# Performance work log

Measured on AMD Instinct MI355X. Metric: run time of the kernel, lower is better.

Reference implementation:

```python
import jax, jax.numpy as jnp
import numpy as np

N_NODES = 100000
N_EDGES = 1600000
D_IN = 128
D_H = 128
NUM_GRAPHS = 128


def setup_inputs() -> dict:
    key = jax.random.key(0)
    ks = jax.random.split(key, 16)
    x = jax.random.normal(ks[0], (N_NODES, D_IN), dtype=jnp.float32)
    edge_index = jax.random.randint(ks[1], (2, N_EDGES), 0, N_NODES, dtype=jnp.int64)
    batch_index = jnp.sort(jax.random.randint(ks[2], (N_NODES,), 0, NUM_GRAPHS, dtype=jnp.int64))
    s = 0.05
    W1 = s * jax.random.normal(ks[3], (D_IN, D_H), dtype=jnp.float32)
    b1 = jnp.zeros((D_H,), jnp.float32)
    W2 = s * jax.random.normal(ks[4], (D_H, D_H), dtype=jnp.float32)
    b2 = jnp.zeros((D_H,), jnp.float32)
    W3 = s * jax.random.normal(ks[5], (D_H, D_H), dtype=jnp.float32)
    b3 = jnp.zeros((D_H,), jnp.float32)
    W4 = s * jax.random.normal(ks[6], (D_H, D_H), dtype=jnp.float32)
    b4 = jnp.zeros((D_H,), jnp.float32)
    Wl = s * jax.random.normal(ks[7], (2 * D_H, 1), dtype=jnp.float32)
    bl = jnp.zeros((1,), jnp.float32)
    return {"x": x, "edge_index": edge_index, "batch_index": batch_index,
            "W1": W1, "b1": b1, "W2": W2, "b2": b2, "W3": W3, "b3": b3,
            "W4": W4, "b4": b4, "Wl": Wl, "bl": bl}


def _gcn_prep(edge_index, n_nodes):
    # add self-loops, symmetric normalization D^-1/2 (A+I) D^-1/2
    loops = jnp.arange(n_nodes, dtype=edge_index.dtype)
    row = jnp.concatenate([edge_index[0], loops])  # source
    col = jnp.concatenate([edge_index[1], loops])  # target
    deg = jax.ops.segment_sum(jnp.ones_like(col, dtype=jnp.float32), col,
                              num_segments=n_nodes)
    dinv = jnp.where(deg > 0, jax.lax.rsqrt(jnp.maximum(deg, 1.0)), 0.0)
    norm = dinv[row] * dinv[col]  # [E+N]
    return row, col, norm


def _gcn(h, W, b, row, col, norm, n_nodes):
    h = h @ W                                   # [N, H]
    msg = h[row] * norm[:, None]                # gather + scale
    return jax.ops.segment_sum(msg, col, num_segments=n_nodes) + b


def reference(x, edge_index, batch_index, W1, b1, W2, b2, W3, b3, W4, b4, Wl, bl):
    n = x.shape[0]
    row, col, norm = _gcn_prep(edge_index, n)
    h = jnp.tanh(_gcn(x, W1, b1, row, col, norm, n))
    h = jnp.tanh(_gcn(h, W2, b2, row, col, norm, n))
    h = jnp.tanh(_gcn(h, W3, b3, row, col, norm, n))
    h = jnp.tanh(_gcn(h, W4, b4, row, col, norm, n))
    # global max / mean pool per graph
    cnt = jax.ops.segment_sum(jnp.ones((n,), jnp.float32), batch_index,
                              num_segments=NUM_GRAPHS)
    mx = jax.ops.segment_max(h, batch_index, num_segments=NUM_GRAPHS)
    mx = jnp.where(cnt[:, None] > 0, mx, 0.0)
    sm = jax.ops.segment_sum(h, batch_index, num_segments=NUM_GRAPHS)
    mn = sm / jnp.maximum(cnt, 1.0)[:, None]
    pooled = jnp.concatenate([mx, mn], axis=1)  # [G, 2H]
    return pooled @ Wl + bl                     # [G, 1]
```

## Files before the change

kernel.cpp:

```cpp
#include <hip/hip_runtime.h>
#include <hip/hip_bf16.h>
#include <math.h>

#define PSPLIT 8
#define BSH 5
#define BW 32
#define AST 40

typedef float v4f __attribute__((ext_vector_type(4)));
typedef unsigned int v4u __attribute__((ext_vector_type(4)));
typedef unsigned int v2u __attribute__((ext_vector_type(2)));
typedef __attribute__((ext_vector_type(8))) short bf8;
typedef __attribute__((ext_vector_type(4))) float f4;
typedef unsigned short u16;
typedef unsigned int u32;

static inline size_t align_up(size_t x, size_t a){ return (x + a - 1) & ~(a - 1); }

__device__ inline void bf_split(float v, u16& hi, u16& lo){
  __hip_bfloat16 h = __float2bfloat16(v);
  float hf = __bfloat162float(h);
  __hip_bfloat16 l = __float2bfloat16(v - hf);
  hi = *(u16*)&h; lo = *(u16*)&l;
}

__device__ inline void fmixlo(float& a, u32 p){
  asm("v_fma_mix_f32 %0, %1, 1.0, %0 op_sel:[0,0,0] op_sel_hi:[1,0,0]" : "+v"(a) : "v"(p));
}
__device__ inline void fmixhi(float& a, u32 p){
  asm("v_fma_mix_f32 %0, %1, 1.0, %0 op_sel:[1,0,0] op_sel_hi:[1,0,0]" : "+v"(a) : "v"(p));
}


__global__ __launch_bounds__(256) void k_bhist(const int* __restrict__ col, int* __restrict__ bcnt,
                                               int E, int NB,
                                               const int* __restrict__ batch, int* __restrict__ gstart,
                                               int n, int G){
  extern __shared__ int lh[];
  for (int i = threadIdx.x; i < NB; i += 256) lh[i] = 0;
  __syncthreads();
  for (int e = blockIdx.x * 256 + threadIdx.x; e < E; e += gridDim.x * 256)
    atomicAdd(&lh[col[e] >> BSH], 1);
  __syncthreads();
  for (int i = threadIdx.x; i < NB; i += 256){
    int v = lh[i];
    if (v) atomicAdd(&bcnt[i], v);
  }
  for (int i = blockIdx.x * 256 + threadIdx.x; i < n; i += gridDim.x * 256){
    int cb = batch[i];
    if (i == 0){ for (int g = 0; g <= cb; ++g) gstart[g] = 0; }
    else { int pb = batch[i - 1]; for (int g = pb + 1; g <= cb; ++g) gstart[g] = i; }
    if (i == n - 1){ for (int g = cb + 1; g <= G; ++g) gstart[g] = n; }
  }
}

__global__ void k_bscan(const int* __restrict__ bcnt, int* __restrict__ boff, int NB, int E,
                        int* __restrict__ rp, int N){
  __shared__ int sd[256];
  int t = threadIdx.x;
  int c[16]; int s = 0;
  const int PT = (NB + 255) / 256;
  for (int j = 0; j < PT; ++j){ int i = t * PT + j; c[j] = (i < NB) ? bcnt[i] : 0; s += c[j]; }
  sd[t] = s; __syncthreads();
  for (int off = 1; off < 256; off <<= 1){
    int v = sd[t];
    if (t >= off) v += sd[t - off];
    __syncthreads(); sd[t] = v; __syncthreads();
  }
  int run = sd[t] - s;
  for (int j = 0; j < PT; ++j){ int i = t * PT + j; if (i < NB) boff[i] = run; run += c[j]; }
  if (t == 255){ boff[NB] = run; rp[N] = E; }
}

__global__ __launch_bounds__(256) void k_bscat(const int* __restrict__ ei, const int* __restrict__ boff,
                                               int* __restrict__ bfill, unsigned* __restrict__ tmp, int E){
  int e = blockIdx.x * 256 + threadIdx.x;
  if (e >= E) return;
  int s = ei[e], d = ei[E + e];
  int b = d >> BSH;
  int p = atomicAdd(&bfill[b * 32], 1);
  tmp[boff[b] + p] = (unsigned)s | ((unsigned)(d & (BW - 1)) << 17);
}

__global__ __launch_bounds__(256) void k_bfin(const unsigned* __restrict__ tmp, const int* __restrict__ boff,
                                              int* __restrict__ ssrc, int* __restrict__ rp,
                                              float* __restrict__ dinv, int N){
  int b = blockIdx.x;
  int d0 = b << BSH;
  int lim = N - d0; if (lim > BW) lim = BW;
  __shared__ int dcnt[BW], dst_[BW], lfill[BW];
  int t = threadIdx.x;
  if (t < BW){ dcnt[t] = 0; lfill[t] = 0; }
  __syncthreads();
  int lo = boff[b], hi = boff[b + 1];
  for (int i = lo + t; i < hi; i += 256) atomicAdd(&dcnt[tmp[i] >> 17], 1);
  __syncthreads();
  if (t == 0){ int run = 0; for (int l = 0; l < BW; ++l){ dst_[l] = run; run += dcnt[l]; } }
  __syncthreads();
  if (t < lim){
    int d = d0 + t;
    rp[d] = lo + dst_[t];
    double dd = (double)(dcnt[t] + 1);
    dinv[d] = (float)(1.0 / sqrt(dd));
  }
  __syncthreads();
  for (int i = lo + t; i < hi; i += 256){
    unsigned r = tmp[i];
    int l = r >> 17;
    int pos = dst_[l] + atomicAdd(&lfill[l], 1);
    ssrc[lo + pos] = (int)(r & 0x1FFFFu);
  }
}


__global__ __launch_bounds__(256) void k_cvtw(const float* __restrict__ w0, const float* __restrict__ w1,
                                              const float* __restrict__ w2, const float* __restrict__ w3,
                                              u16* __restrict__ wth, u16* __restrict__ wtl){
  int id = blockIdx.x * 256 + threadIdx.x;
  if (id >= 4 * 16384) return;
  int l = id >> 14, rem = id & 16383, k = rem >> 7, nn = rem & 127;
  const float* Wsrc = (l == 0) ? w0 : (l == 1) ? w1 : (l == 2) ? w2 : w3;
  float v = Wsrc[k * 128 + nn];
  u16 hi, lo; bf_split(v, hi, lo);
  wth[(l << 14) + nn * 128 + k] = hi;
  wtl[(l << 14) + nn * 128 + k] = lo;
}


__global__ __launch_bounds__(256, 4) void k_gemm(const float* __restrict__ A,
                                                 const u16* __restrict__ wth, const u16* __restrict__ wtl,
                                                 const float* __restrict__ dinv,
                                                 u16* __restrict__ C, int n, int packed){
  __shared__ u16 Ah[128 * AST], Al[128 * AST], Wh[128 * AST], Wl[128 * AST];
  int t = threadIdx.x;
  int r0 = blockIdx.x * 128;
  int wv = t >> 6, lane = t & 63;
  int q = lane >> 4, ln = lane & 15;

  int srow = t >> 1;
  int shalf = (t & 1) * 16;
  int grow = r0 + srow; if (grow > n - 1) grow = n - 1;
  const float* ga = A + (size_t)grow * 128 + shalf;
  const u16* gwh = wth + srow * 128 + shalf;
  const u16* gwl = wtl + srow * 128 + shalf;

  f4 acc[2][8];
  #pragma unroll
  for (int mt = 0; mt < 2; ++mt)
    #pragma unroll
    for (int nt = 0; nt < 8; ++nt) acc[mt][nt] = (f4)(0.f);

  for (int c = 0; c < 4; ++c){
    __syncthreads();
    {
      u16* ah = &Ah[srow * AST + shalf];
      u16* al = &Al[srow * AST + shalf];
      if (packed){
        const v4u* gp = (const v4u*)(ga + c * 32);
        #pragma unroll
        for (int i = 0; i < 4; ++i){
          v4u v = gp[i];
          ushort4 hv = {(u16)(v.x >> 16), (u16)(v.y >> 16), (u16)(v.z >> 16), (u16)(v.w >> 16)};
          ushort4 lv = {(u16)v.x, (u16)v.y, (u16)v.z, (u16)v.w};
          *(ushort4*)&ah[i * 4] = hv;
          *(ushort4*)&al[i * 4] = lv;
        }
      } else {
        const float4* gp = (const float4*)(ga + c * 32);
        #pragma unroll
        for (int i = 0; i < 4; ++i){
          float4 v = gp[i];
          u16 h0,h1,h2,h3,l0,l1,l2,l3;
          bf_split(v.x, h0, l0); bf_split(v.y, h1, l1);
          bf_split(v.z, h2, l2); bf_split(v.w, h3, l3);
          ushort4 hv = {h0,h1,h2,h3}, lv = {l0,l1,l2,l3};
          *(ushort4*)&ah[i * 4] = hv;
          *(ushort4*)&al[i * 4] = lv;
        }
      }
    }
    {
      const u16* ph = gwh + c * 32;
      const u16* pl = gwl + c * 32;
      bf8 h0 = *(const bf8*)ph, h1 = *(const bf8*)(ph + 8);
      bf8 l0 = *(const bf8*)pl, l1 = *(const bf8*)(pl + 8);
      *(bf8*)&Wh[srow * AST + shalf] = h0; *(bf8*)&Wh[srow * AST + shalf + 8] = h1;
      *(bf8*)&Wl[srow * AST + shalf] = l0; *(bf8*)&Wl[srow * AST + shalf + 8] = l1;
    }
    __syncthreads();

    bf8 afh[2], afl[2];
    #pragma unroll
    for (int mt = 0; mt < 2; ++mt){
      int row = wv * 32 + mt * 16 + ln;
      afh[mt] = *(const bf8*)&Ah[row * AST + q * 8];
      afl[mt] = *(const bf8*)&Al[row * AST + q * 8];
    }
    #pragma unroll
    for (int nt = 0; nt < 8; ++nt){
      int wn = nt * 16 + ln;
      bf8 wfh = *(const bf8*)&Wh[wn * AST + q * 8];
      bf8 wfl = *(const bf8*)&Wl[wn * AST + q * 8];
      #pragma unroll
      for (int mt = 0; mt < 2; ++mt){
        acc[mt][nt] = __builtin_amdgcn_mfma_f32_16x16x32_bf16(afh[mt], wfh, acc[mt][nt], 0, 0, 0);
        acc[mt][nt] = __builtin_amdgcn_mfma_f32_16x16x32_bf16(afl[mt], wfh, acc[mt][nt], 0, 0, 0);
        acc[mt][nt] = __builtin_amdgcn_mfma_f32_16x16x32_bf16(afh[mt], wfl, acc[mt][nt], 0, 0, 0);
      }
    }
  }

  #pragma unroll
  for (int mt = 0; mt < 2; ++mt){
    int base_m = r0 + wv * 32 + mt * 16 + q * 4;
    float dv[4];
    #pragma unroll
    for (int reg = 0; reg < 4; ++reg){
      int row = base_m + reg;
      dv[reg] = (row < n) ? dinv[row] : 0.f;
    }
    #pragma unroll
    for (int nt = 0; nt < 8; ++nt){
      #pragma unroll
      for (int reg = 0; reg < 4; ++reg){
        int row = base_m + reg;
        if (row < n){
          _Float16 hv = (_Float16)(acc[mt][nt][reg] * dv[reg]);
          C[(size_t)row * 128 + nt * 16 + ln] = *(u16*)&hv;
        }
      }
    }
  }
}


__global__ __launch_bounds__(256) void k_agg(const u16* __restrict__ hwp, const int* __restrict__ rp,
                                             const int* __restrict__ ssrc,
                                             const float* __restrict__ dinv, const float* __restrict__ bias,
                                             float* __restrict__ hout, int n, int pack){
  int b = blockIdx.x;
  int r = b & 7;
  int F = r >> 2;
  int s = (b >> 3) * 4 + (r & 3);
  int node = s * 4 + (threadIdx.x >> 6);
  if (node >= n) return;
  int lane = threadIdx.x & 63;
  int ql = lane >> 4;
  int fl = lane & 15;
  const char* hbase = (const char*)(hwp + F * 64);
  u32 flb = (u32)fl * 8;

  int e0 = rp[node], e1 = rp[node + 1];
  float a0 = 0.f, a1 = 0.f, a2 = 0.f, a3 = 0.f;
  for (int eb = e0; eb < e1; eb += 64){
    int m = e1 - eb; if (m > 64) m = 64;
    int sl = (lane < m) ? ssrc[eb + lane] : 0;
    int mp = m & ~3;
    int j = 0;
    for (; j + 16 <= mp; j += 16){
      int s0 = __shfl(sl, j + ql),     s1 = __shfl(sl, j + 4 + ql);
      int s2 = __shfl(sl, j + 8 + ql), s3 = __shfl(sl, j + 12 + ql);
      v2u v0 = *(const v2u*)(hbase + (((u32)s0 << 8) + flb));
      v2u v1 = *(const v2u*)(hbase + (((u32)s1 << 8) + flb));
      v2u v2_ = *(const v2u*)(hbase + (((u32)s2 << 8) + flb));
      v2u v3 = *(const v2u*)(hbase + (((u32)s3 << 8) + flb));
      fmixlo(a0, v0.x); fmixhi(a1, v0.x); fmixlo(a2, v0.y); fmixhi(a3, v0.y);
      fmixlo(a0, v1.x); fmixhi(a1, v1.x); fmixlo(a2, v1.y); fmixhi(a3, v1.y);
      fmixlo(a0, v2_.x); fmixhi(a1, v2_.x); fmixlo(a2, v2_.y); fmixhi(a3, v2_.y);
      fmixlo(a0, v3.x); fmixhi(a1, v3.x); fmixlo(a2, v3.y); fmixhi(a3, v3.y);
    }
    if (j + 8 <= mp){
      int s0 = __shfl(sl, j + ql), s1 = __shfl(sl, j + 4 + ql);
      v2u v0 = *(const v2u*)(hbase + (((u32)s0 << 8) + flb));
      v2u v1 = *(const v2u*)(hbase + (((u32)s1 << 8) + flb));
      fmixlo(a0, v0.x); fmixhi(a1, v0.x); fmixlo(a2, v0.y); fmixhi(a3, v0.y);
      fmixlo(a0, v1.x); fmixhi(a1, v1.x); fmixlo(a2, v1.y); fmixhi(a3, v1.y);
      j += 8;
    }
    if (j + 4 <= mp){
      int s0 = __shfl(sl, j + ql);
      v2u v0 = *(const v2u*)(hbase + (((u32)s0 << 8) + flb));
      fmixlo(a0, v0.x); fmixhi(a1, v0.x); fmixlo(a2, v0.y); fmixhi(a3, v0.y);
      j += 4;
    }
    if (j < m){
      int s0 = __shfl(sl, j + ql);
      if (j + ql < m){
        v2u v0 = *(const v2u*)(hbase + (((u32)s0 << 8) + flb));
        fmixlo(a0, v0.x); fmixhi(a1, v0.x); fmixlo(a2, v0.y); fmixhi(a3, v0.y);
      }
    }
  }
  a0 += __shfl_down(a0, 32); a1 += __shfl_down(a1, 32);
  a2 += __shfl_down(a2, 32); a3 += __shfl_down(a3, 32);
  a0 += __shfl_down(a0, 16); a1 += __shfl_down(a1, 16);
  a2 += __shfl_down(a2, 16); a3 += __shfl_down(a3, 16);
  if (lane < 16){
    v2u sv = *(const v2u*)(hbase + (((u32)node << 8) + flb));
    fmixlo(a0, sv.x); fmixhi(a1, sv.x); fmixlo(a2, sv.y); fmixhi(a3, sv.y);
    float di = dinv[node];
    int f = F * 64 + fl * 4;
    v4f bv = *(const v4f*)(bias + f);
    float r0 = tanhf(a0 * di + bv.x);
    float r1 = tanhf(a1 * di + bv.y);
    float r2 = tanhf(a2 * di + bv.z);
    float r3 = tanhf(a3 * di + bv.w);
    if (pack){
      u16 h0,h1,h2,h3,l0,l1,l2,l3;
      bf_split(r0, h0, l0); bf_split(r1, h1, l1);
      bf_split(r2, h2, l2); bf_split(r3, h3, l3);
      v4u pv;
      pv.x = ((u32)h0 << 16) | l0; pv.y = ((u32)h1 << 16) | l1;
      pv.z = ((u32)h2 << 16) | l2; pv.w = ((u32)h3 << 16) | l3;
      __builtin_nontemporal_store(pv, (v4u*)(hout + (size_t)node * 128 + f));
    } else {
      v4f rr; rr.x = r0; rr.y = r1; rr.z = r2; rr.w = r3;
      __builtin_nontemporal_store(rr, (v4f*)(hout + (size_t)node * 128 + f));
    }
  }
}


__global__ __launch_bounds__(256) void k_pool1(const float* __restrict__ h, const int* __restrict__ gstart,
                                               float* __restrict__ pmx, float* __restrict__ psm){
  int g = blockIdx.x >> 3, s = blockIdx.x & (PSPLIT - 1);
  int t = threadIdx.x;
  int fq = t & 31;
  int rw = t >> 5;
  int i0 = gstart[g], i1 = gstart[g + 1];
  int len = i1 - i0;
  int chunk = (len + PSPLIT - 1) / PSPLIT;
  int a = i0 + s * chunk;
  int b = a + chunk; if (b > i1) b = i1;

  const v4f* hv = (const v4f*)h;
  v4f mx = (v4f)(-INFINITY), sm = (v4f)(0.f);
  for (int i = a + rw; i < b; i += 8){
    v4f v = hv[(size_t)i * 32 + fq];
    mx.x = fmaxf(mx.x, v.x); mx.y = fmaxf(mx.y, v.y);
    mx.z = fmaxf(mx.z, v.z); mx.w = fmaxf(mx.w, v.w);
    sm += v;
  }
  __shared__ v4f smx[8][32], ssm[8][32];
  smx[rw][fq] = mx; ssm[rw][fq] = sm;
  __syncthreads();
  if (rw == 0){
    #pragma unroll
    for (int r2 = 1; r2 < 8; ++r2){
      v4f m2 = smx[r2][fq], s2 = ssm[r2][fq];
      mx.x = fmaxf(mx.x, m2.x); mx.y = fmaxf(mx.y, m2.y);
      mx.z = fmaxf(mx.z, m2.z); mx.w = fmaxf(mx.w, m2.w);
      sm += s2;
    }
    ((v4f*)pmx)[(size_t)blockIdx.x * 32 + fq] = mx;
    ((v4f*)psm)[(size_t)blockIdx.x * 32 + fq] = sm;
  }
}

__global__ __launch_bounds__(128) void k_head(const float* __restrict__ pmx, const float* __restrict__ psm,
                                              const int* __restrict__ gstart,
                                              const float* __restrict__ Wl, const float* __restrict__ bl,
                                              float* __restrict__ out){
  int g = blockIdx.x, f = threadIdx.x;
  float mx = -INFINITY, sm = 0.f;
  #pragma unroll
  for (int s = 0; s < PSPLIT; ++s){
    mx = fmaxf(mx, pmx[((size_t)g * PSPLIT + s) * 128 + f]);
    sm += psm[((size_t)g * PSPLIT + s) * 128 + f];
  }
  int cnt = gstart[g + 1] - gstart[g];
  if (cnt <= 0) mx = 0.f;
  float mn = sm / (float)(cnt > 0 ? cnt : 1);
  float contrib = mx * Wl[f] + mn * Wl[128 + f];
  for (int o = 32; o > 0; o >>= 1) contrib += __shfl_down(contrib, o);
  __shared__ float sred[2];
  if ((f & 63) == 0) sred[f >> 6] = contrib;
  __syncthreads();
  if (f == 0) out[g] = sred[0] + sred[1] + bl[0];
}


extern "C" void kernel_launch(void* const* d_in, const int* in_sizes, int n_in,
                              void* d_out, int out_size, void* d_ws, size_t ws_size,
                              hipStream_t stream){
  const float* x     = (const float*)d_in[0];
  const int*   ei    = (const int*)d_in[1];
  const int*   batch = (const int*)d_in[2];
  const float* W[4]  = {(const float*)d_in[3], (const float*)d_in[5], (const float*)d_in[7], (const float*)d_in[9]};
  const float* B[4]  = {(const float*)d_in[4], (const float*)d_in[6], (const float*)d_in[8], (const float*)d_in[10]};
  const float* Wl    = (const float*)d_in[11];
  const float* bl    = (const float*)d_in[12];
  float* out = (float*)d_out;

  int N = in_sizes[0] / 128;
  int E = in_sizes[1] / 2;
  int G = out_size;
  int NB = (N + BW - 1) >> BSH;

  char* ws = (char*)d_ws;
  size_t off = 0;
  auto alloc = [&](size_t bytes) -> void* {
    void* p = ws + off; off = align_up(off + bytes, 256); return p;
  };
  float* dinv  = (float*)alloc((size_t)N * 4);
  int*   rp    = (int*)  alloc((size_t)(N + 1) * 4);
  int*   bcnt  = (int*)  alloc((size_t)(NB + 1) * 4);
  int*   boff  = (int*)  alloc((size_t)(NB + 1) * 4);
  int*   bfill = (int*)  alloc((size_t)NB * 32 * 4);
  int*   gst   = (int*)  alloc((size_t)(G + 1) * 4);
  int*   ssrc  = (int*)  alloc((size_t)E * 4);
  u16*   wth   = (u16*)  alloc((size_t)4 * 16384 * 2);
  u16*   wtl   = (u16*)  alloc((size_t)4 * 16384 * 2);
  float* pmx   = (float*)alloc((size_t)G * PSPLIT * 128 * 4);
  float* psm   = (float*)alloc((size_t)G * PSPLIT * 128 * 4);
  u16*   hw    = (u16*)  alloc((size_t)N * 128 * 2);
  float* h     = (float*)alloc((size_t)N * 128 * 4);
  unsigned* tmp = (unsigned*)hw;

  hipMemsetAsync(bcnt, 0, (size_t)(NB + 1) * 4, stream);
  hipMemsetAsync(bfill, 0, (size_t)NB * 32 * 4, stream);

  int gE = (E + 255) / 256;
  k_cvtw <<<256, 256, 0, stream>>>(W[0], W[1], W[2], W[3], wth, wtl);
  k_bhist<<<128, 256, NB * 4, stream>>>(ei + E, bcnt, E, NB, batch, gst, N, G);
  k_bscan<<<1, 256, 0, stream>>>(bcnt, boff, NB, E, rp, N);
  k_bscat<<<gE, 256, 0, stream>>>(ei, boff, bfill, tmp, E);
  k_bfin <<<NB, 256, 0, stream>>>(tmp, boff, ssrc, rp, dinv, N);

  int gemmG = (N + 127) / 128;
  int slots = (N + 3) / 4;
  int aggG  = 8 * ((slots + 3) / 4);
  const float* hin = x;
  for (int l = 0; l < 4; ++l){
    k_gemm<<<gemmG, 256, 0, stream>>>(hin, wth + (l << 14), wtl + (l << 14), dinv, hw, N, l > 0);
    k_agg <<<aggG, 256, 0, stream>>>(hw, rp, ssrc, dinv, B[l], h, N, l < 3);
    hin = h;
  }
  k_pool1<<<G * PSPLIT, 256, 0, stream>>>(h, gst, pmx, psm);
  k_head <<<G, 128, 0, stream>>>(pmx, psm, gst, Wl, bl, out);
}
```

Baseline: 655.0 us.

## Restructure aggregation to one wave per node over all features with fast tanh

The aggregation kernel now assigns one 64-lane wave to each node, with every lane covering two features of the full 128-wide row. Previously sixteen lanes each covered four features of one 64-feature half, and four edge groups ran in parallel and were combined by shuffle reductions. The new layout removes the feature split across blocks, the shuffle-based index broadcast and the reductions. Neighbour indices are read as wave-uniform scalar loads, and edges are unrolled by 16 to keep many row gathers in flight. tanhf is replaced by an exp2/rcp approximation, which is cheaper but may lose some accuracy and could overflow for large inputs.

After: 579.6 us. 1.13x faster.

```diff
diff --git a/kernel.cpp b/kernel.cpp
--- a/kernel.cpp
+++ b/kernel.cpp
@@ -8,6 +8,7 @@
 #define AST 40
 
 typedef float v4f __attribute__((ext_vector_type(4)));
+typedef float v2f __attribute__((ext_vector_type(2)));
 typedef unsigned int v4u __attribute__((ext_vector_type(4)));
 typedef unsigned int v2u __attribute__((ext_vector_type(2)));
 typedef __attribute__((ext_vector_type(8))) short bf8;
@@ -29,6 +30,12 @@
 }
 __device__ inline void fmixhi(float& a, u32 p){
   asm("v_fma_mix_f32 %0, %1, 1.0, %0 op_sel:[1,0,0] op_sel_hi:[1,0,0]" : "+v"(a) : "v"(p));
+}
+
+__device__ inline float tanh_fast(float x){
+  float u = __builtin_amdgcn_exp2f(x * 2.8853900817779268f);
+  float q = __builtin_amdgcn_rcpf(u + 1.0f);
+  return fmaf(-2.0f, q, 1.0f);
 }
 
 
@@ -238,85 +245,61 @@
                                              const int* __restrict__ ssrc,
                                              const float* __restrict__ dinv, const float* __restrict__ bias,
                                              float* __restrict__ hout, int n, int pack){
-  int b = blockIdx.x;
-  int r = b & 7;
-  int F = r >> 2;
-  int s = (b >> 3) * 4 + (r & 3);
-  int node = s * 4 + (threadIdx.x >> 6);
+  int node = blockIdx.x * 4 + (threadIdx.x >> 6);
+  node = __builtin_amdgcn_readfirstlane(node);
   if (node >= n) return;
   int lane = threadIdx.x & 63;
-  int ql = lane >> 4;
-  int fl = lane & 15;
-  const char* hbase = (const char*)(hwp + F * 64);
-  u32 flb = (u32)fl * 8;
+  const u32* hw32 = (const u32*)hwp;
 
   int e0 = rp[node], e1 = rp[node + 1];
-  float a0 = 0.f, a1 = 0.f, a2 = 0.f, a3 = 0.f;
-  for (int eb = e0; eb < e1; eb += 64){
-    int m = e1 - eb; if (m > 64) m = 64;
-    int sl = (lane < m) ? ssrc[eb + lane] : 0;
-    int mp = m & ~3;
-    int j = 0;
-    for (; j + 16 <= mp; j += 16){
-      int s0 = __shfl(sl, j + ql),     s1 = __shfl(sl, j + 4 + ql);
-      int s2 = __shfl(sl, j + 8 + ql), s3 = __shfl(sl, j + 12 + ql);
-      v2u v0 = *(const v2u*)(hbase + (((u32)s0 << 8) + flb));
-      v2u v1 = *(const v2u*)(hbase + (((u32)s1 << 8) + flb));
-      v2u v2_ = *(const v2u*)(hbase + (((u32)s2 << 8) + flb));
-      v2u v3 = *(const v2u*)(hbase + (((u32)s3 << 8) + flb));
-      fmixlo(a0, v0.x); fmixhi(a1, v0.x); fmixlo(a2, v0.y); fmixhi(a3, v0.y);
-      fmixlo(a0, v1.x); fmixhi(a1, v1.x); fmixlo(a2, v1.y); fmixhi(a3, v1.y);
-      fmixlo(a0, v2_.x); fmixhi(a1, v2_.x); fmixlo(a2, v2_.y); fmixhi(a3, v2_.y);
-      fmixlo(a0, v3.x); fmixhi(a1, v3.x); fmixlo(a2, v3.y); fmixhi(a3, v3.y);
-    }
-    if (j + 8 <= mp){
-      int s0 = __shfl(sl, j + ql), s1 = __shfl(sl, j + 4 + ql);
-      v2u v0 = *(const v2u*)(hbase + (((u32)s0 << 8) + flb));
-      v2u v1 = *(const v2u*)(hbase + (((u32)s1 << 8) + flb));
-      fmixlo(a0, v0.x); fmixhi(a1, v0.x); fmixlo(a2, v0.y); fmixhi(a3, v0.y);
-      fmixlo(a0, v1.x); fmixhi(a1, v1.x); fmixlo(a2, v1.y); fmixhi(a3, v1.y);
-      j += 8;
-    }
-    if (j + 4 <= mp){
-      int s0 = __shfl(sl, j + ql);
-      v2u v0 = *(const v2u*)(hbase + (((u32)s0 << 8) + flb));
-      fmixlo(a0, v0.x); fmixhi(a1, v0.x); fmixlo(a2, v0.y); fmixhi(a3, v0.y);
-      j += 4;
-    }
-    if (j < m){
-      int s0 = __shfl(sl, j + ql);
-      if (j + ql < m){
-        v2u v0 = *(const v2u*)(hbase + (((u32)s0 << 8) + flb));
-        fmixlo(a0, v0.x); fmixhi(a1, v0.x); fmixlo(a2, v0.y); fmixhi(a3, v0.y);
-      }
-    }
-  }
-  a0 += __shfl_down(a0, 32); a1 += __shfl_down(a1, 32);
-  a2 += __shfl_down(a2, 32); a3 += __shfl_down(a3, 32);
-  a0 += __shfl_down(a0, 16); a1 += __shfl_down(a1, 16);
-  a2 += __shfl_down(a2, 16); a3 += __shfl_down(a3, 16);
-  if (lane < 16){
-    v2u sv = *(const v2u*)(hbase + (((u32)node << 8) + flb));
-    fmixlo(a0, sv.x); fmixhi(a1, sv.x); fmixlo(a2, sv.y); fmixhi(a3, sv.y);
-    float di = dinv[node];
-    int f = F * 64 + fl * 4;
-    v4f bv = *(const v4f*)(bias + f);
-    float r0 = tanhf(a0 * di + bv.x);
-    float r1 = tanhf(a1 * di + bv.y);
-    float r2 = tanhf(a2 * di + bv.z);
-    float r3 = tanhf(a3 * di + bv.w);
-    if (pack){
-      u16 h0,h1,h2,h3,l0,l1,l2,l3;
-      bf_split(r0, h0, l0); bf_split(r1, h1, l1);
-      bf_split(r2, h2, l2); bf_split(r3, h3, l3);
-      v4u pv;
-      pv.x = ((u32)h0 << 16) | l0; pv.y = ((u32)h1 << 16) | l1;
-      pv.z = ((u32)h2 << 16) | l2; pv.w = ((u32)h3 << 16) | l3;
-      __builtin_nontemporal_store(pv, (v4u*)(hout + (size_t)node * 128 + f));
-    } else {
-      v4f rr; rr.x = r0; rr.y = r1; rr.z = r2; rr.w = r3;
-      __builtin_nontemporal_store(rr, (v4f*)(hout + (size_t)node * 128 + f));
-    }
+  float a0 = 0.f, a1 = 0.f;
+  int e = e0;
+  while (e + 16 <= e1){
+    u32 p[16];
+    #pragma unroll
+    for (int i = 0; i < 16; ++i){
+      int s = ssrc[e + i];
+      p[i] = hw32[(size_t)s * 64 + lane];
+    }
+    #pragma unroll
+    for (int i = 0; i < 16; ++i){ fmixlo(a0, p[i]); fmixhi(a1, p[i]); }
+    e += 16;
+  }
+  while (e + 4 <= e1){
+    u32 p[4];
+    #pragma unroll
+    for (int i = 0; i < 4; ++i){
+      int s = ssrc[e + i];
+      p[i] = hw32[(size_t)s * 64 + lane];
+    }
+    #pragma unroll
+    for (int i = 0; i < 4; ++i){ fmixlo(a0, p[i]); fmixhi(a1, p[i]); }
+    e += 4;
+  }
+  while (e < e1){
+    int s = ssrc[e];
+    u32 p = hw32[(size_t)s * 64 + lane];
+    fmixlo(a0, p); fmixhi(a1, p);
+    ++e;
+  }
+  {
+    u32 p = hw32[(size_t)node * 64 + lane];
+    fmixlo(a0, p); fmixhi(a1, p);
+  }
+  float di = dinv[node];
+  v2f bv = *(const v2f*)(bias + lane * 2);
+  float r0 = tanh_fast(fmaf(a0, di, bv.x));
+  float r1 = tanh_fast(fmaf(a1, di, bv.y));
+  if (pack){
+    u16 h0, h1, l0, l1;
+    bf_split(r0, h0, l0); bf_split(r1, h1, l1);
+    v2u pv;
+    pv.x = ((u32)h0 << 16) | l0;
+    pv.y = ((u32)h1 << 16) | l1;
+    __builtin_nontemporal_store(pv, (v2u*)((u32*)hout + (size_t)node * 128 + lane * 2));
+  } else {
+    v2f rr; rr.x = r0; rr.y = r1;
+    __builtin_nontemporal_store(rr, (v2f*)(hout + (size_t)node * 128 + lane * 2));
   }
 }
 
@@ -428,8 +411,7 @@
   k_bfin <<<NB, 256, 0, stream>>>(tmp, boff, ssrc, rp, dinv, N);
 
   int gemmG = (N + 127) / 128;
-  int slots = (N + 3) / 4;
-  int aggG  = 8 * ((slots + 3) / 4);
+  int aggG  = (N + 3) / 4;
   const float* hin = x;
   for (int l = 0; l < 4; ++l){
     k_gemm<<<gemmG, 256, 0, stream>>>(hin, wth + (l << 14), wtl + (l << 14), dinv, hw, N, l > 0);
```
